# Kernel tuning notes

Measured on AMD Instinct MI355X. Metric: run time of the kernel, lower is better.

The kernel has to match this reference:

```python
import jax, jax.numpy as jnp
import numpy as np

N = 262144      # total nodes
E = 1048576     # total edges
G = 8192        # num graphs (= batch[-1]+1)
H = 128         # hidden
L = 4           # layers
VA = 64         # atom feature vocab
VB = 8          # bond feature vocab
FA = 9          # atom feature columns
FB = 3          # bond feature columns
BN_EPS = 1e-5


def _bn(x, g, b, m, v):
    # BatchNorm1d in eval mode: running stats
    return (x - m) * jax.lax.rsqrt(v + BN_EPS) * g + b


def setup_inputs() -> dict:
    key = jax.random.key(0)
    ks = jax.random.split(key, 40)
    rn = lambda k, s, sc=0.05: jax.random.normal(k, s, dtype=jnp.float32) * sc
    x = jax.random.randint(ks[0], (N, FA), 0, VA)
    edge_index = jax.random.randint(ks[1], (2, E), 0, N)
    edge_attr = jax.random.randint(ks[2], (E, FB), 0, VB)
    batch = jnp.sort(jax.random.randint(ks[3], (N,), 0, G))
    batch = batch.at[0].set(0).at[-1].set(G - 1)
    params = dict(
        atom_emb=rn(ks[4], (FA, VA, H)),
        vn_emb=rn(ks[5], (H,)),
        bond_emb=rn(ks[6], (L, FB, VB, H)),
        conv_eps=rn(ks[7], (L,)),
        conv_W1=rn(ks[8], (L, H, 2 * H)), conv_b1=rn(ks[9], (L, 2 * H)),
        conv_bn_g=1.0 + rn(ks[10], (L, 2 * H)), conv_bn_b=rn(ks[11], (L, 2 * H)),
        conv_bn_m=rn(ks[12], (L, 2 * H), 0.1),
        conv_bn_v=0.5 + jax.random.uniform(ks[13], (L, 2 * H)) * 0.5,
        conv_W2=rn(ks[14], (L, 2 * H, H)), conv_b2=rn(ks[15], (L, H)),
        vn1_W=rn(ks[16], (L, 2 * H, 2 * H)), vn1_b=rn(ks[17], (L, 2 * H)),
        vn1_g=1.0 + rn(ks[18], (L, 2 * H)), vn1_be=rn(ks[19], (L, 2 * H)),
        vn1_m=rn(ks[20], (L, 2 * H), 0.1),
        vn1_v=0.5 + jax.random.uniform(ks[21], (L, 2 * H)) * 0.5,
        vn2_W=rn(ks[22], (L, 2 * H, H)), vn2_b=rn(ks[23], (L, H)),
        vn2_g=1.0 + rn(ks[24], (L, H)), vn2_be=rn(ks[25], (L, H)),
        vn2_m=rn(ks[26], (L, H), 0.1),
        vn2_v=0.5 + jax.random.uniform(ks[27], (L, H)) * 0.5,
        pW1=rn(ks[28], (H, H)), pb1=rn(ks[29], (H,)),
        pW2=rn(ks[30], (H, 1)), pb2=rn(ks[31], (1,)),
    )
    return dict(x=x, edge_index=edge_index, edge_attr=edge_attr, batch=batch, **params)


def reference(x, edge_index, edge_attr, batch, atom_emb, vn_emb, bond_emb,
              conv_eps, conv_W1, conv_b1, conv_bn_g, conv_bn_b, conv_bn_m, conv_bn_v,
              conv_W2, conv_b2, vn1_W, vn1_b, vn1_g, vn1_be, vn1_m, vn1_v,
              vn2_W, vn2_b, vn2_g, vn2_be, vn2_m, vn2_v, pW1, pb1, pW2, pb2):
    src, dst = edge_index[0], edge_index[1]
    # AtomEncoder: sum of per-feature embeddings -> [N, H]
    h = atom_emb[jnp.arange(FA)[:, None], x.T].sum(0)
    # virtual node embedding broadcast to all graphs: [G, H]
    vn = jnp.broadcast_to(vn_emb, (G, H))
    for i in range(L):
        h = h + vn[batch]
        # CombConv (GIN-with-edge-features): msg = relu(x_j + bond_emb)
        e = bond_emb[i][jnp.arange(FB)[:, None], edge_attr.T].sum(0)  # [E, H]
        msg = jax.nn.relu(h[src] + e)
        agg = jax.ops.segment_sum(msg, dst, num_segments=N)  # [N, H]
        z = (1.0 + conv_eps[i]) * h + agg
        z = jax.nn.relu(_bn(z @ conv_W1[i] + conv_b1[i],
                            conv_bn_g[i], conv_bn_b[i], conv_bn_m[i], conv_bn_v[i]))
        h = z @ conv_W2[i] + conv_b2[i]
        # virtual node update: gather-concat-MLP, pool, MLP
        t = jnp.concatenate([vn[batch], h], axis=-1)  # [N, 2H]
        t = jax.nn.relu(_bn(t @ vn1_W[i] + vn1_b[i],
                            vn1_g[i], vn1_be[i], vn1_m[i], vn1_v[i]))
        pooled = jax.ops.segment_sum(t, batch, num_segments=G)  # [G, 2H]
        vn = jax.nn.relu(_bn(pooled @ vn2_W[i] + vn2_b[i],
                             vn2_g[i], vn2_be[i], vn2_m[i], vn2_v[i]))
    # JK='L': last virtual-node representation; dropout=0
    out = jax.nn.relu(vn @ pW1 + pb1) @ pW2 + pb2  # [G, 1]
    return jnp.clip(out, 0.0, 50.0)  # eval-mode clamp
```

## Files before the change

kernel.cpp:

```cpp
#include <hip/hip_runtime.h>
#include <hip/hip_fp16.h>

#define NN 262144
#define EE 1048576
#define GG 8192
#define HH 128
#define FBc 3
#define VAc 64
#define VBc 8
#define FAc 9

typedef _Float16 f16;
typedef _Float16 f16x8 __attribute__((ext_vector_type(8)));
typedef float f32x4 __attribute__((ext_vector_type(4)));

__device__ __forceinline__ float h2f(ushort u) {
    __half h; *(ushort*)&h = u; return __half2float(h);
}
__device__ __forceinline__ ushort f2h(float f) {
    __half h = __float2half_rn(f); return *(ushort*)&h;
}

__global__ void k_zero(float* __restrict__ p) {
    size_t i = (size_t)(blockIdx.x * 256 + threadIdx.x) * 4;
    *(float4*)(p + i) = make_float4(0.f, 0.f, 0.f, 0.f);
}

__global__ void k_atom(const int* __restrict__ x, const float* __restrict__ emb,
                       ushort* __restrict__ h16) {
    int t = blockIdx.x * 256 + threadIdx.x;
    int n = t >> 5, c = (t & 31) << 2;
    if (n >= NN) return;
    float4 a = make_float4(0.f, 0.f, 0.f, 0.f);
#pragma unroll
    for (int f = 0; f < FAc; ++f) {
        int v = x[n * FAc + f];
        float4 e = *(const float4*)(emb + ((size_t)(f * VAc + v)) * HH + c);
        a.x += e.x; a.y += e.y; a.z += e.z; a.w += e.w;
    }
    ushort4 o;
    o.x = f2h(a.x * 0.0625f); o.y = f2h(a.y * 0.0625f);
    o.z = f2h(a.z * 0.0625f); o.w = f2h(a.w * 0.0625f);
    *(ushort4*)(h16 + (size_t)n * HH + c) = o;
}

__global__ void k_init_vn(const float* __restrict__ vn_emb, float* __restrict__ vn) {
    int t = blockIdx.x * 256 + threadIdx.x;
    int g = t >> 5, c = (t & 31) << 2;
    *(float4*)(vn + (size_t)g * HH + c) = *(const float4*)(vn_emb + c);
}

__global__ void k_vn16(const float* __restrict__ vn, ushort* __restrict__ vn16) {
    int t = blockIdx.x * 256 + threadIdx.x;
    float4 v = *(const float4*)(vn + (size_t)t * 4);
    ushort4 o;
    o.x = f2h(v.x * 0.0625f); o.y = f2h(v.y * 0.0625f);
    o.z = f2h(v.z * 0.0625f); o.w = f2h(v.w * 0.0625f);
    *(ushort4*)(vn16 + (size_t)t * 4) = o;
}

__global__ void k_hist(const int* __restrict__ ei, int* __restrict__ deg) {
    int e = blockIdx.x * 256 + threadIdx.x;
    atomicAdd(&deg[ei[EE + e]], 1);
}
__global__ void k_scan1(const int* __restrict__ deg, int* __restrict__ rowptr,
                        int* __restrict__ sums) {
    __shared__ int s[256];
    int base = blockIdx.x * 1024 + threadIdx.x * 4;
    int4 d = *(const int4*)(deg + base);
    int t = d.x + d.y + d.z + d.w;
    s[threadIdx.x] = t;
    __syncthreads();
    for (int off = 1; off < 256; off <<= 1) {
        int v = (threadIdx.x >= off) ? s[threadIdx.x - off] : 0;
        __syncthreads();
        s[threadIdx.x] += v;
        __syncthreads();
    }
    int excl = s[threadIdx.x] - t;
    int4 o; o.x = excl; o.y = excl + d.x; o.z = o.y + d.y; o.w = o.z + d.z;
    *(int4*)(rowptr + base) = o;
    if (threadIdx.x == 255) sums[blockIdx.x] = s[255];
}
__global__ void k_scan2(int* __restrict__ sums) {
    __shared__ int s[256];
    int t = sums[threadIdx.x];
    s[threadIdx.x] = t;
    __syncthreads();
    for (int off = 1; off < 256; off <<= 1) {
        int v = (threadIdx.x >= off) ? s[threadIdx.x - off] : 0;
        __syncthreads();
        s[threadIdx.x] += v;
        __syncthreads();
    }
    sums[threadIdx.x] = s[threadIdx.x] - t;
}
__global__ void k_scan3(int* __restrict__ rowptr, const int* __restrict__ sums,
                        int* __restrict__ fill) {
    int base = blockIdx.x * 1024 + threadIdx.x * 4;
    int add = sums[blockIdx.x];
    int4 r = *(const int4*)(rowptr + base);
    r.x += add; r.y += add; r.z += add; r.w += add;
    *(int4*)(rowptr + base) = r;
    *(int4*)(fill + base) = r;
    if (blockIdx.x == 0 && threadIdx.x == 0) rowptr[NN] = EE;
}
__global__ void k_scatter(const int* __restrict__ ei, const int* __restrict__ ea,
                          int* __restrict__ fill, unsigned* __restrict__ packed) {
    int e = blockIdx.x * 256 + threadIdx.x;
    int dst = ei[EE + e];
    int pos = atomicAdd(&fill[dst], 1);
    unsigned cb = (unsigned)(ea[e * 3 + 0] + ea[e * 3 + 1] * 8 + ea[e * 3 + 2] * 64);
    packed[pos] = (unsigned)ei[e] | (cb << 18);
}

__global__ void k_ctab(const float* __restrict__ bemb, float* __restrict__ ctab) {
    int t = blockIdx.x * 256 + threadIdx.x;
    int cb = t >> 5, c = (t & 31) << 2;
    int a0 = cb & 7, a1 = (cb >> 3) & 7, a2 = cb >> 6;
    float4 b0 = *(const float4*)(bemb + (size_t)(0 * VBc + a0) * HH + c);
    float4 b1 = *(const float4*)(bemb + (size_t)(1 * VBc + a1) * HH + c);
    float4 b2 = *(const float4*)(bemb + (size_t)(2 * VBc + a2) * HH + c);
    float4 o = make_float4(b0.x + b1.x + b2.x, b0.y + b1.y + b2.y,
                           b0.z + b1.z + b2.z, b0.w + b1.w + b2.w);
    *(float4*)(ctab + (size_t)cb * HH + c) = o;
}

__global__ void k_prep(const float* __restrict__ b1, const float* __restrict__ g1,
                       const float* __restrict__ be1, const float* __restrict__ m1,
                       const float* __restrict__ v1,
                       const float* __restrict__ g3, const float* __restrict__ be3,
                       const float* __restrict__ m3, const float* __restrict__ v3,
                       float* __restrict__ ZA, float* __restrict__ ZB,
                       float* __restrict__ TA, float* __restrict__ TB,
                       float* __restrict__ S3) {
    int c = threadIdx.x;
    float s1 = g1[c] * rsqrtf(v1[c] + 1e-5f);
    ZA[c] = s1;
    ZB[c] = ((b1[c] - m1[c]) * s1 + be1[c]) * 0.0625f;
    float s3 = g3[c] * rsqrtf(v3[c] + 1e-5f);
    TA[c] = 16.f * s3;
    TB[c] = be3[c] - m3[c] * s3;
    S3[c] = s3;
}

__global__ void k_wt(const float* __restrict__ W, ushort* __restrict__ Wt, int lk, int Nsrc) {
    int o = blockIdx.x * 256 + threadIdx.x;
    int K = 1 << lk;
    int c = o >> lk, k = o & (K - 1);
    Wt[o] = f2h(W[(size_t)k * Nsrc + c]);
}

__global__ void k_agg(const ushort* __restrict__ h16, const ushort* __restrict__ vn16,
                      const int* __restrict__ batch,
                      const int* __restrict__ rowptr, const unsigned* __restrict__ packed,
                      const float* __restrict__ ctab, ushort* __restrict__ agg) {
    int n = blockIdx.x * 4 + (threadIdx.x >> 6);
    int lane = threadIdx.x & 63;
    int co = lane * 2;
    int beg = rowptr[n], end = rowptr[n + 1];
    float a0 = 0.f, a1 = 0.f;
    int i = beg;
    for (; i + 1 < end; i += 2) {
        unsigned p0 = packed[i], p1 = packed[i + 1];
        int s0 = p0 & 0x3FFFF, s1 = p1 & 0x3FFFF;
        int c0 = p0 >> 18, c1 = p1 >> 18;
        ushort2 u0 = *(const ushort2*)(h16 + (size_t)s0 * HH + co);
        ushort2 u1 = *(const ushort2*)(h16 + (size_t)s1 * HH + co);
        ushort2 w0 = *(const ushort2*)(vn16 + (size_t)batch[s0] * HH + co);
        ushort2 w1 = *(const ushort2*)(vn16 + (size_t)batch[s1] * HH + co);
        float2 t0 = *(const float2*)(ctab + (size_t)c0 * HH + co);
        float2 t1 = *(const float2*)(ctab + (size_t)c1 * HH + co);
        a0 += fmaxf(16.f * (h2f(u0.x) + h2f(w0.x)) + t0.x, 0.f)
            + fmaxf(16.f * (h2f(u1.x) + h2f(w1.x)) + t1.x, 0.f);
        a1 += fmaxf(16.f * (h2f(u0.y) + h2f(w0.y)) + t0.y, 0.f)
            + fmaxf(16.f * (h2f(u1.y) + h2f(w1.y)) + t1.y, 0.f);
    }
    if (i < end) {
        unsigned p = packed[i];
        int src = p & 0x3FFFF, cb = p >> 18;
        ushort2 u = *(const ushort2*)(h16 + (size_t)src * HH + co);
        ushort2 wv = *(const ushort2*)(vn16 + (size_t)batch[src] * HH + co);
        float2 ct = *(const float2*)(ctab + (size_t)cb * HH + co);
        a0 += fmaxf(16.f * (h2f(u.x) + h2f(wv.x)) + ct.x, 0.f);
        a1 += fmaxf(16.f * (h2f(u.y) + h2f(wv.y)) + ct.y, 0.f);
    }
    ushort2 o; o.x = f2h(a0 * 0.0625f); o.y = f2h(a1 * 0.0625f);
    *(ushort2*)(agg + (size_t)n * HH + co) = o;
}

__global__ void __launch_bounds__(256, 2)
k_conv(ushort* __restrict__ h16, const ushort* __restrict__ agg,
       const ushort* __restrict__ W1t, const ushort* __restrict__ W2t,
       const ushort* __restrict__ W3t,
       const int* __restrict__ batch, const ushort* __restrict__ vn16,
       const float* __restrict__ vnW,
       const float* __restrict__ eps_ptr,
       const float* __restrict__ ZA, const float* __restrict__ ZB,
       const float* __restrict__ b2,
       const float* __restrict__ TA, const float* __restrict__ TB,
       float* __restrict__ pooled) {
    __shared__ ushort As[64][128];
    __shared__ ushort zs[64][256];
    __shared__ ushort Wb[64][256];
    ushort(*Wq)[128] = (ushort(*)[128]) & Wb[0][0];
    const int tid = threadIdx.x;
    const int r0 = blockIdx.x * 64;
    const int w = tid >> 6, l = tid & 63, lr = l & 15, lg = l >> 4, lr7 = lr & 7;
    const float eps1 = 1.f + eps_ptr[0];
    f32x4 acc[4];

    {
        int row = tid >> 2, q = tid & 3, r7 = row & 7;
        int gg = batch[r0 + row];
        const ushort* hp = h16 + (size_t)(r0 + row) * HH;
        const ushort* vp = vn16 + (size_t)gg * HH;
        const ushort* ap = agg + (size_t)(r0 + row) * HH;
#pragma unroll
        for (int j4 = 0; j4 < 4; ++j4) {
            int c0 = q * 32 + j4 * 8;
            f16x8 hv = *(const f16x8*)(hp + c0);
            f16x8 vg = *(const f16x8*)(vp + c0);
            f16x8 ag = *(const f16x8*)(ap + c0);
            f16x8 o;
#pragma unroll
            for (int j = 0; j < 8; ++j)
                o[j] = (f16)(eps1 * ((float)hv[j] + (float)vg[j]) + (float)ag[j]);
            *(f16x8*)&As[row][((c0 >> 3) ^ r7) << 3] = o;
        }
    }

    for (int qt = 0; qt < 4; ++qt) {
        __syncthreads();
        {
            int c = tid >> 2, q = tid & 3, c7 = c & 7;
#pragma unroll
            for (int j4 = 0; j4 < 4; ++j4) {
                int blk = q * 4 + j4;
                *(f16x8*)&Wq[c][(blk ^ c7) << 3] =
                    *(const f16x8*)(W1t + (size_t)(qt * 64 + c) * 128 + blk * 8);
            }
        }
        __syncthreads();
#pragma unroll
        for (int fc = 0; fc < 4; ++fc) acc[fc] = (f32x4){0.f, 0.f, 0.f, 0.f};
#pragma unroll
        for (int k0 = 0; k0 < 4; ++k0) {
            int sb = ((k0 * 4 + lg) ^ lr7) << 3;
            f16x8 af = *(const f16x8*)&As[w * 16 + lr][sb];
#pragma unroll
            for (int fc = 0; fc < 4; ++fc) {
                f16x8 bf = *(const f16x8*)&Wq[fc * 16 + lr][sb];
                acc[fc] = __builtin_amdgcn_mfma_f32_16x16x32_f16(af, bf, acc[fc], 0, 0, 0);
            }
        }
#pragma unroll
        for (int fc = 0; fc < 4; ++fc) {
            int col = qt * 64 + fc * 16 + lr;
            float za = ZA[col], zb = ZB[col];
#pragma unroll
            for (int reg = 0; reg < 4; ++reg) {
                int rl = w * 16 + lg * 4 + reg;
                float zv = fmaxf(acc[fc][reg] * za + zb, 0.f);
                zs[rl][(((col >> 3) ^ (rl & 7)) << 3) | (col & 7)] = f2h(zv);
            }
        }
    }

    for (int ch = 0; ch < 2; ++ch) {
        __syncthreads();
        {
            int c = tid >> 2, q = tid & 3, c7 = c & 7;
#pragma unroll
            for (int j8 = 0; j8 < 8; ++j8) {
                int blk = q * 8 + j8;
                *(f16x8*)&Wb[c][(blk ^ c7) << 3] =
                    *(const f16x8*)(W2t + (size_t)(ch * 64 + c) * 256 + blk * 8);
            }
        }
        __syncthreads();
#pragma unroll
        for (int fc = 0; fc < 4; ++fc) acc[fc] = (f32x4){0.f, 0.f, 0.f, 0.f};
#pragma unroll
        for (int k0 = 0; k0 < 8; ++k0) {
            int sb = ((k0 * 4 + lg) ^ lr7) << 3;
            f16x8 af = *(const f16x8*)&zs[w * 16 + lr][sb];
#pragma unroll
            for (int fc = 0; fc < 4; ++fc) {
                f16x8 bf = *(const f16x8*)&Wb[fc * 16 + lr][sb];
                acc[fc] = __builtin_amdgcn_mfma_f32_16x16x32_f16(af, bf, acc[fc], 0, 0, 0);
            }
        }
#pragma unroll
        for (int fc = 0; fc < 4; ++fc) {
            int col = ch * 64 + fc * 16 + lr;
            float bb = b2[col];
#pragma unroll
            for (int reg = 0; reg < 4; ++reg) {
                int rl = w * 16 + lg * 4 + reg;
                float hv = acc[fc][reg] * 16.f + bb;
                ushort hq = f2h(hv * 0.0625f);
                h16[(size_t)(r0 + rl) * HH + col] = hq;
                As[rl][(((col >> 3) ^ (rl & 7)) << 3) | (col & 7)] = hq;
            }
        }
    }

    for (int qt = 0; qt < 4; ++qt) {
        __syncthreads();
        {
            int c = tid >> 2, q = tid & 3, c7 = c & 7;
#pragma unroll
            for (int j4 = 0; j4 < 4; ++j4) {
                int blk = q * 4 + j4;
                *(f16x8*)&Wq[c][(blk ^ c7) << 3] =
                    *(const f16x8*)(W3t + (size_t)(qt * 64 + c) * 128 + blk * 8);
            }
        }
        __syncthreads();
#pragma unroll
        for (int fc = 0; fc < 4; ++fc) acc[fc] = (f32x4){0.f, 0.f, 0.f, 0.f};
#pragma unroll
        for (int k0 = 0; k0 < 4; ++k0) {
            int sb = ((k0 * 4 + lg) ^ lr7) << 3;
            f16x8 af = *(const f16x8*)&As[w * 16 + lr][sb];
#pragma unroll
            for (int fc = 0; fc < 4; ++fc) {
                f16x8 bf = *(const f16x8*)&Wq[fc * 16 + lr][sb];
                acc[fc] = __builtin_amdgcn_mfma_f32_16x16x32_f16(af, bf, acc[fc], 0, 0, 0);
            }
        }
        int rls[4], ggs[4];
#pragma unroll
        for (int reg = 0; reg < 4; ++reg) {
            rls[reg] = w * 16 + lg * 4 + reg;
            ggs[reg] = batch[r0 + rls[reg]];
        }
#pragma unroll
        for (int fc = 0; fc < 4; ++fc) {
            int colg = qt * 64 + fc * 16 + lr;
            float ta = TA[colg], tb = TB[colg];
#pragma unroll
            for (int reg = 0; reg < 4; ++reg) {
                int rl = rls[reg];
                float tv = fmaxf(acc[fc][reg] * ta + vnW[(size_t)ggs[reg] * 256 + colg] + tb, 0.f);
                zs[rl][(((colg >> 3) ^ (rl & 7)) << 3) | (colg & 7)] = f2h(tv);
            }
        }
    }
    __syncthreads();
    {
        int col = tid;
        float s = 0.f;
        int cur = batch[r0];
        for (int r = 0; r < 64; ++r) {
            int gg = batch[r0 + r];
            if (gg != cur) {
                atomicAdd(&pooled[(size_t)cur * 256 + col], s);
                s = 0.f; cur = gg;
            }
            s += h2f(zs[r][(((col >> 3) ^ (r & 7)) << 3) | (col & 7)]);
        }
        atomicAdd(&pooled[(size_t)cur * 256 + col], s);
    }
}

enum { E_BIAS = 0, E_BNRELU = 1 };
template <int EMODE>
__global__ void __launch_bounds__(256)
gemm_k(const void* __restrict__ Av, const float* __restrict__ B,
       const float* __restrict__ bias,
       const float* __restrict__ g_, const float* __restrict__ b_,
       const float* __restrict__ m_, const float* __restrict__ v_,
       const float* __restrict__ scp,
       void* __restrict__ outv, int K, int Nc) {
    __shared__ float As[64][33];
    __shared__ float Bs[32][64];
    const int tid = threadIdx.x;
    const int row0 = blockIdx.x * 64;
    const int col0 = blockIdx.y * 64;
    float acc[4][4] = {};
    const int tx = tid & 15, ty = tid >> 4;
    for (int k0 = 0; k0 < K; k0 += 32) {
#pragma unroll
        for (int p = 0; p < 2; ++p) {
            int idx = p * 256 + tid;
            {
                int r = idx >> 3, c = (idx & 7) << 2;
                size_t aoff = (size_t)(row0 + r) * K + k0 + c;
                float4 va = *(const float4*)((const float*)Av + aoff);
                As[r][c + 0] = va.x; As[r][c + 1] = va.y;
                As[r][c + 2] = va.z; As[r][c + 3] = va.w;
            }
            {
                int kr = idx >> 4, cc = (idx & 15) << 2;
                *(float4*)&Bs[kr][cc] =
                    *(const float4*)(B + (size_t)(k0 + kr) * Nc + col0 + cc);
            }
        }
        __syncthreads();
#pragma unroll
        for (int k = 0; k < 32; ++k) {
            float4 bv = *(const float4*)&Bs[k][tx << 2];
            float a0 = As[ty * 4 + 0][k];
            float a1 = As[ty * 4 + 1][k];
            float a2 = As[ty * 4 + 2][k];
            float a3 = As[ty * 4 + 3][k];
            acc[0][0] += a0 * bv.x; acc[0][1] += a0 * bv.y; acc[0][2] += a0 * bv.z; acc[0][3] += a0 * bv.w;
            acc[1][0] += a1 * bv.x; acc[1][1] += a1 * bv.y; acc[1][2] += a1 * bv.z; acc[1][3] += a1 * bv.w;
            acc[2][0] += a2 * bv.x; acc[2][1] += a2 * bv.y; acc[2][2] += a2 * bv.z; acc[2][3] += a2 * bv.w;
            acc[3][0] += a3 * bv.x; acc[3][1] += a3 * bv.y; acc[3][2] += a3 * bv.z; acc[3][3] += a3 * bv.w;
        }
        __syncthreads();
    }
#pragma unroll
    for (int j = 0; j < 4; ++j) {
        int gr = row0 + ty * 4 + j;
        float vals[4];
#pragma unroll
        for (int lx = 0; lx < 4; ++lx) {
            int gc = col0 + (tx << 2) + lx;
            float val = acc[j][lx];
            if (EMODE == E_BIAS) {
                float v = val + bias[gc];
                if (scp) v *= scp[gc];
                vals[lx] = v;
            } else {
                float y = val + bias[gc];
                float s = g_[gc] * rsqrtf(v_[gc] + 1e-5f);
                y = (y - m_[gc]) * s + b_[gc];
                vals[lx] = fmaxf(y, 0.f);
            }
        }
        *(float4*)((float*)outv + (size_t)gr * Nc + col0 + (tx << 2)) =
            make_float4(vals[0], vals[1], vals[2], vals[3]);
    }
}

__global__ void k_final(const float* __restrict__ vn, const float* __restrict__ pW1,
                        const float* __restrict__ pb1, const float* __restrict__ pW2,
                        const float* __restrict__ pb2, float* __restrict__ out) {
    int g = blockIdx.x;
    int j = threadIdx.x;
    __shared__ float vrow[HH];
    __shared__ float red[HH];
    vrow[j] = vn[(size_t)g * HH + j];
    __syncthreads();
    float acc = pb1[j];
    for (int k = 0; k < HH; ++k) acc = fmaf(vrow[k], pW1[k * HH + j], acc);
    red[j] = fmaxf(acc, 0.f) * pW2[j];
    __syncthreads();
    for (int s = 64; s > 0; s >>= 1) {
        if (j < s) red[j] += red[j + s];
        __syncthreads();
    }
    if (j == 0) out[g] = fminf(fmaxf(red[0] + pb2[0], 0.f), 50.f);
}

extern "C" void kernel_launch(void* const* d_in, const int* in_sizes, int n_in,
                              void* d_out, int out_size, void* d_ws, size_t ws_size,
                              hipStream_t stream) {
    const int*   x        = (const int*)  d_in[0];
    const int*   ei       = (const int*)  d_in[1];
    const int*   ea       = (const int*)  d_in[2];
    const int*   batch    = (const int*)  d_in[3];
    const float* atom_emb = (const float*)d_in[4];
    const float* vn_emb   = (const float*)d_in[5];
    const float* bond_emb = (const float*)d_in[6];
    const float* conv_eps = (const float*)d_in[7];
    const float* conv_W1  = (const float*)d_in[8];
    const float* conv_b1  = (const float*)d_in[9];
    const float* cbn_g    = (const float*)d_in[10];
    const float* cbn_b    = (const float*)d_in[11];
    const float* cbn_m    = (const float*)d_in[12];
    const float* cbn_v    = (const float*)d_in[13];
    const float* conv_W2  = (const float*)d_in[14];
    const float* conv_b2  = (const float*)d_in[15];
    const float* vn1_W    = (const float*)d_in[16];
    const float* vn1_b    = (const float*)d_in[17];
    const float* vn1_g    = (const float*)d_in[18];
    const float* vn1_be   = (const float*)d_in[19];
    const float* vn1_m    = (const float*)d_in[20];
    const float* vn1_v    = (const float*)d_in[21];
    const float* vn2_W    = (const float*)d_in[22];
    const float* vn2_b    = (const float*)d_in[23];
    const float* vn2_g    = (const float*)d_in[24];
    const float* vn2_be   = (const float*)d_in[25];
    const float* vn2_m    = (const float*)d_in[26];
    const float* vn2_v    = (const float*)d_in[27];
    const float* pW1      = (const float*)d_in[28];
    const float* pb1      = (const float*)d_in[29];
    const float* pW2      = (const float*)d_in[30];
    const float* pb2      = (const float*)d_in[31];

    char* base = (char*)d_ws;
    ushort*   h16    = (ushort*)base;
    ushort*   agg    = h16 + (size_t)NN * HH;
    unsigned* packed = (unsigned*)(agg + (size_t)NN * HH);
    int*      rowptr = (int*)(packed + EE);
    int*      fill   = rowptr + NN + 4;
    float*    ctab   = (float*)(fill + NN);
    int*      sums   = (int*)(ctab + 512 * HH);
    ushort*   W1t    = (ushort*)(sums + 256);
    ushort*   W2t    = W1t + 256 * 128;
    ushort*   W3t    = W2t + 128 * 256;
    float*    ZA     = (float*)(W3t + 256 * 128);
    float*    ZB     = ZA + 256;
    float*    TA     = ZB + 256;
    float*    TB     = TA + 256;
    float*    S3     = TB + 256;
    float*    vn     = S3 + 256;
    ushort*   vn16   = (ushort*)(vn + (size_t)GG * HH);
    float*    vnW    = (float*)(vn16 + (size_t)GG * HH);
    float*    pooled = vnW + (size_t)GG * 256;
    float*    out    = (float*)d_out;

    k_zero<<<256, 256, 0, stream>>>((float*)fill);
    k_hist<<<EE / 256, 256, 0, stream>>>(ei, fill);
    k_scan1<<<256, 256, 0, stream>>>(fill, rowptr, sums);
    k_scan2<<<1, 256, 0, stream>>>(sums);
    k_scan3<<<256, 256, 0, stream>>>(rowptr, sums, fill);
    k_scatter<<<EE / 256, 256, 0, stream>>>(ei, ea, fill, packed);
    k_atom<<<NN * 32 / 256, 256, 0, stream>>>(x, atom_emb, h16);
    k_init_vn<<<GG * HH / 4 / 256, 256, 0, stream>>>(vn_emb, vn);

    for (int i = 0; i < 4; ++i) {
        k_ctab<<<64, 256, 0, stream>>>(bond_emb + (size_t)i * FBc * VBc * HH, ctab);
        k_prep<<<1, 256, 0, stream>>>(
            conv_b1 + i * 256, cbn_g + i * 256, cbn_b + i * 256,
            cbn_m + i * 256, cbn_v + i * 256,
            vn1_g + i * 256, vn1_be + i * 256, vn1_m + i * 256, vn1_v + i * 256,
            ZA, ZB, TA, TB, S3);
        k_wt<<<128, 256, 0, stream>>>(conv_W1 + (size_t)i * HH * 256, W1t, 7, 256);
        k_wt<<<128, 256, 0, stream>>>(conv_W2 + (size_t)i * 256 * HH, W2t, 8, 128);
        k_wt<<<128, 256, 0, stream>>>(vn1_W + (size_t)i * 256 * 256 + 128 * 256, W3t, 7, 256);
        k_vn16<<<GG * HH / 4 / 256, 256, 0, stream>>>(vn, vn16);

        k_agg<<<NN / 4, 256, 0, stream>>>(h16, vn16, batch, rowptr, packed, ctab, agg);

        {
            dim3 g3(GG / 64, 4);
            gemm_k<E_BIAS><<<g3, 256, 0, stream>>>(
                vn, vn1_W + (size_t)i * 256 * 256, vn1_b + i * 256,
                nullptr, nullptr, nullptr, nullptr, S3, vnW, HH, 256);
        }
        k_zero<<<GG * 256 / 4 / 256, 256, 0, stream>>>(pooled);

        k_conv<<<NN / 64, 256, 0, stream>>>(
            h16, agg, W1t, W2t, W3t, batch, vn16, vnW, conv_eps + i,
            ZA, ZB, conv_b2 + i * HH, TA, TB, pooled);

        {
            dim3 g4(GG / 64, 2);
            gemm_k<E_BNRELU><<<g4, 256, 0, stream>>>(
                pooled, vn2_W + (size_t)i * 256 * HH, vn2_b + i * HH,
                vn2_g + i * HH, vn2_be + i * HH, vn2_m + i * HH, vn2_v + i * HH,
                nullptr, vn, 256, HH);
        }
    }
    k_final<<<GG, 128, 0, stream>>>(vn, pW1, pb1, pW2, pb2, out);
}
```

Baseline: 1.609 ms.

## Read conv weights directly from global and shrink LDS to raise occupancy

Rewrites the fused conv kernel so the MFMA B-operands come straight from global or L2 instead of being staged through shared memory. A-fragments for the first GEMM are built in registers, and one 64x256 LDS buffer is reused for z, h and the t halves. The pooling reduction is split into two halves of columns, each with its own barrier. This removes most __syncthreads and LDS traffic and raises the occupancy target to 4 blocks per CU, at the cost of redundant per-wave weight reads from cache and more register pressure (8 accumulators for the second GEMM).

After: 2.742 ms. 1.7x slower.

```diff
diff --git a/kernel.cpp b/kernel.cpp
--- a/kernel.cpp
+++ b/kernel.cpp
@@ -189,7 +189,7 @@
     *(ushort2*)(agg + (size_t)n * HH + co) = o;
 }
 
-__global__ void __launch_bounds__(256, 2)
+__global__ void __launch_bounds__(256, 4)
 k_conv(ushort* __restrict__ h16, const ushort* __restrict__ agg,
        const ushort* __restrict__ W1t, const ushort* __restrict__ W2t,
        const ushort* __restrict__ W3t,
@@ -200,58 +200,44 @@
        const float* __restrict__ b2,
        const float* __restrict__ TA, const float* __restrict__ TB,
        float* __restrict__ pooled) {
-    __shared__ ushort As[64][128];
     __shared__ ushort zs[64][256];
-    __shared__ ushort Wb[64][256];
-    ushort(*Wq)[128] = (ushort(*)[128]) & Wb[0][0];
     const int tid = threadIdx.x;
     const int r0 = blockIdx.x * 64;
     const int w = tid >> 6, l = tid & 63, lr = l & 15, lg = l >> 4, lr7 = lr & 7;
     const float eps1 = 1.f + eps_ptr[0];
-    f32x4 acc[4];
-
-    {
-        int row = tid >> 2, q = tid & 3, r7 = row & 7;
-        int gg = batch[r0 + row];
-        const ushort* hp = h16 + (size_t)(r0 + row) * HH;
-        const ushort* vp = vn16 + (size_t)gg * HH;
-        const ushort* ap = agg + (size_t)(r0 + row) * HH;
-#pragma unroll
-        for (int j4 = 0; j4 < 4; ++j4) {
-            int c0 = q * 32 + j4 * 8;
-            f16x8 hv = *(const f16x8*)(hp + c0);
-            f16x8 vg = *(const f16x8*)(vp + c0);
-            f16x8 ag = *(const f16x8*)(ap + c0);
-            f16x8 o;
-#pragma unroll
-            for (int j = 0; j < 8; ++j)
-                o[j] = (f16)(eps1 * ((float)hv[j] + (float)vg[j]) + (float)ag[j]);
-            *(f16x8*)&As[row][((c0 >> 3) ^ r7) << 3] = o;
-        }
-    }
-
+    const int myrow = w * 16 + lr;
+    const int growA = r0 + myrow;
+    const int ggA = batch[growA];
+    int rl[4], ggs[4];
+#pragma unroll
+    for (int reg = 0; reg < 4; ++reg) {
+        rl[reg] = w * 16 + lg * 4 + reg;
+        ggs[reg] = batch[r0 + rl[reg]];
+    }
+
+    f16x8 af[4];
+#pragma unroll
+    for (int k0 = 0; k0 < 4; ++k0) {
+        int ko = k0 * 32 + lg * 8;
+        f16x8 hv = *(const f16x8*)(h16 + (size_t)growA * HH + ko);
+        f16x8 vv = *(const f16x8*)(vn16 + (size_t)ggA * HH + ko);
+        f16x8 ag = *(const f16x8*)(agg + (size_t)growA * HH + ko);
+#pragma unroll
+        for (int j = 0; j < 8; ++j)
+            af[k0][j] = (f16)(eps1 * ((float)hv[j] + (float)vv[j]) + (float)ag[j]);
+    }
+
+#pragma unroll
     for (int qt = 0; qt < 4; ++qt) {
-        __syncthreads();
-        {
-            int c = tid >> 2, q = tid & 3, c7 = c & 7;
-#pragma unroll
-            for (int j4 = 0; j4 < 4; ++j4) {
-                int blk = q * 4 + j4;
-                *(f16x8*)&Wq[c][(blk ^ c7) << 3] =
-                    *(const f16x8*)(W1t + (size_t)(qt * 64 + c) * 128 + blk * 8);
-            }
-        }
-        __syncthreads();
-#pragma unroll
-        for (int fc = 0; fc < 4; ++fc) acc[fc] = (f32x4){0.f, 0.f, 0.f, 0.f};
+        f32x4 acc[4] = {};
 #pragma unroll
         for (int k0 = 0; k0 < 4; ++k0) {
-            int sb = ((k0 * 4 + lg) ^ lr7) << 3;
-            f16x8 af = *(const f16x8*)&As[w * 16 + lr][sb];
+            int ko = k0 * 32 + lg * 8;
 #pragma unroll
             for (int fc = 0; fc < 4; ++fc) {
-                f16x8 bf = *(const f16x8*)&Wq[fc * 16 + lr][sb];
-                acc[fc] = __builtin_amdgcn_mfma_f32_16x16x32_f16(af, bf, acc[fc], 0, 0, 0);
+                int col = qt * 64 + fc * 16 + lr;
+                f16x8 bf = *(const f16x8*)(W1t + (size_t)col * 128 + ko);
+                acc[fc] = __builtin_amdgcn_mfma_f32_16x16x32_f16(af[k0], bf, acc[fc], 0, 0, 0);
             }
         }
 #pragma unroll
@@ -260,108 +246,85 @@
             float za = ZA[col], zb = ZB[col];
 #pragma unroll
             for (int reg = 0; reg < 4; ++reg) {
-                int rl = w * 16 + lg * 4 + reg;
                 float zv = fmaxf(acc[fc][reg] * za + zb, 0.f);
-                zs[rl][(((col >> 3) ^ (rl & 7)) << 3) | (col & 7)] = f2h(zv);
-            }
-        }
-    }
-
-    for (int ch = 0; ch < 2; ++ch) {
+                zs[rl[reg]][(((col >> 3) ^ (rl[reg] & 7)) << 3) | (col & 7)] = f2h(zv);
+            }
+        }
+    }
+
+    {
+        f32x4 acc2[8] = {};
+#pragma unroll
+        for (int k0 = 0; k0 < 8; ++k0) {
+            int ko = k0 * 32 + lg * 8;
+            f16x8 az = *(const f16x8*)&zs[myrow][(((k0 * 4 + lg) ^ lr7)) << 3];
+#pragma unroll
+            for (int ofc = 0; ofc < 8; ++ofc) {
+                int col = (ofc >> 2) * 64 + (ofc & 3) * 16 + lr;
+                f16x8 bf = *(const f16x8*)(W2t + (size_t)col * 256 + ko);
+                acc2[ofc] = __builtin_amdgcn_mfma_f32_16x16x32_f16(az, bf, acc2[ofc], 0, 0, 0);
+            }
+        }
+#pragma unroll
+        for (int ofc = 0; ofc < 8; ++ofc) {
+            int col = (ofc >> 2) * 64 + (ofc & 3) * 16 + lr;
+            float bb = b2[col];
+#pragma unroll
+            for (int reg = 0; reg < 4; ++reg) {
+                float hv = acc2[ofc][reg] * 16.f + bb;
+                ushort hq = f2h(hv * 0.0625f);
+                h16[(size_t)(r0 + rl[reg]) * HH + col] = hq;
+                zs[rl[reg]][(((col >> 3) ^ (rl[reg] & 7)) << 3) | (col & 7)] = hq;
+            }
+        }
+    }
+
+    for (int pr = 0; pr < 2; ++pr) {
+#pragma unroll
+        for (int sub = 0; sub < 2; ++sub) {
+            int qt = pr * 2 + sub;
+            f32x4 acc3[4] = {};
+#pragma unroll
+            for (int k0 = 0; k0 < 4; ++k0) {
+                int ko = k0 * 32 + lg * 8;
+                f16x8 ah = *(const f16x8*)&zs[myrow][(((k0 * 4 + lg) ^ lr7)) << 3];
+#pragma unroll
+                for (int fc = 0; fc < 4; ++fc) {
+                    int col = qt * 64 + fc * 16 + lr;
+                    f16x8 bf = *(const f16x8*)(W3t + (size_t)col * 128 + ko);
+                    acc3[fc] = __builtin_amdgcn_mfma_f32_16x16x32_f16(ah, bf, acc3[fc], 0, 0, 0);
+                }
+            }
+#pragma unroll
+            for (int fc = 0; fc < 4; ++fc) {
+                int colg = qt * 64 + fc * 16 + lr;
+                int colL = 128 + sub * 64 + fc * 16 + lr;
+                float ta = TA[colg], tb = TB[colg];
+#pragma unroll
+                for (int reg = 0; reg < 4; ++reg) {
+                    float tv = fmaxf(acc3[fc][reg] * ta + vnW[(size_t)ggs[reg] * 256 + colg] + tb, 0.f);
+                    zs[rl[reg]][(((colL >> 3) ^ (rl[reg] & 7)) << 3) | (colL & 7)] = f2h(tv);
+                }
+            }
+        }
         __syncthreads();
         {
-            int c = tid >> 2, q = tid & 3, c7 = c & 7;
-#pragma unroll
-            for (int j8 = 0; j8 < 8; ++j8) {
-                int blk = q * 8 + j8;
-                *(f16x8*)&Wb[c][(blk ^ c7) << 3] =
-                    *(const f16x8*)(W2t + (size_t)(ch * 64 + c) * 256 + blk * 8);
-            }
-        }
-        __syncthreads();
-#pragma unroll
-        for (int fc = 0; fc < 4; ++fc) acc[fc] = (f32x4){0.f, 0.f, 0.f, 0.f};
-#pragma unroll
-        for (int k0 = 0; k0 < 8; ++k0) {
-            int sb = ((k0 * 4 + lg) ^ lr7) << 3;
-            f16x8 af = *(const f16x8*)&zs[w * 16 + lr][sb];
-#pragma unroll
-            for (int fc = 0; fc < 4; ++fc) {
-                f16x8 bf = *(const f16x8*)&Wb[fc * 16 + lr][sb];
-                acc[fc] = __builtin_amdgcn_mfma_f32_16x16x32_f16(af, bf, acc[fc], 0, 0, 0);
-            }
-        }
-#pragma unroll
-        for (int fc = 0; fc < 4; ++fc) {
-            int col = ch * 64 + fc * 16 + lr;
-            float bb = b2[col];
-#pragma unroll
-            for (int reg = 0; reg < 4; ++reg) {
-                int rl = w * 16 + lg * 4 + reg;
-                float hv = acc[fc][reg] * 16.f + bb;
-                ushort hq = f2h(hv * 0.0625f);
-                h16[(size_t)(r0 + rl) * HH + col] = hq;
-                As[rl][(((col >> 3) ^ (rl & 7)) << 3) | (col & 7)] = hq;
-            }
-        }
-    }
-
-    for (int qt = 0; qt < 4; ++qt) {
-        __syncthreads();
-        {
-            int c = tid >> 2, q = tid & 3, c7 = c & 7;
-#pragma unroll
-            for (int j4 = 0; j4 < 4; ++j4) {
-                int blk = q * 4 + j4;
-                *(f16x8*)&Wq[c][(blk ^ c7) << 3] =
-                    *(const f16x8*)(W3t + (size_t)(qt * 64 + c) * 128 + blk * 8);
-            }
-        }
-        __syncthreads();
-#pragma unroll
-        for (int fc = 0; fc < 4; ++fc) acc[fc] = (f32x4){0.f, 0.f, 0.f, 0.f};
-#pragma unroll
-        for (int k0 = 0; k0 < 4; ++k0) {
-            int sb = ((k0 * 4 + lg) ^ lr7) << 3;
-            f16x8 af = *(const f16x8*)&As[w * 16 + lr][sb];
-#pragma unroll
-            for (int fc = 0; fc < 4; ++fc) {
-                f16x8 bf = *(const f16x8*)&Wq[fc * 16 + lr][sb];
-                acc[fc] = __builtin_amdgcn_mfma_f32_16x16x32_f16(af, bf, acc[fc], 0, 0, 0);
-            }
-        }
-        int rls[4], ggs[4];
-#pragma unroll
-        for (int reg = 0; reg < 4; ++reg) {
-            rls[reg] = w * 16 + lg * 4 + reg;
-            ggs[reg] = batch[r0 + rls[reg]];
-        }
-#pragma unroll
-        for (int fc = 0; fc < 4; ++fc) {
-            int colg = qt * 64 + fc * 16 + lr;
-            float ta = TA[colg], tb = TB[colg];
-#pragma unroll
-            for (int reg = 0; reg < 4; ++reg) {
-                int rl = rls[reg];
-                float tv = fmaxf(acc[fc][reg] * ta + vnW[(size_t)ggs[reg] * 256 + colg] + tb, 0.f);
-                zs[rl][(((colg >> 3) ^ (rl & 7)) << 3) | (colg & 7)] = f2h(tv);
-            }
-        }
-    }
-    __syncthreads();
-    {
-        int col = tid;
-        float s = 0.f;
-        int cur = batch[r0];
-        for (int r = 0; r < 64; ++r) {
-            int gg = batch[r0 + r];
-            if (gg != cur) {
-                atomicAdd(&pooled[(size_t)cur * 256 + col], s);
-                s = 0.f; cur = gg;
-            }
-            s += h2f(zs[r][(((col >> 3) ^ (r & 7)) << 3) | (col & 7)]);
-        }
-        atomicAdd(&pooled[(size_t)cur * 256 + col], s);
+            int c = tid & 127, half = tid >> 7;
+            int gcol = pr * 128 + c;
+            int colL = 128 + c;
+            float s = 0.f;
+            int cur = batch[r0 + half * 32];
+            for (int r = half * 32; r < half * 32 + 32; ++r) {
+                int gg = batch[r0 + r];
+                if (gg != cur) {
+                    atomicAdd(&pooled[(size_t)cur * 256 + gcol], s);
+                    s = 0.f; cur = gg;
+                }
+                s += h2f(zs[r][(((colL >> 3) ^ (r & 7)) << 3) | (colL & 7)]);
+            }
+            atomicAdd(&pooled[(size_t)cur * 256 + gcol], s);
+        }
+        __syncthreads();
     }
 }
 
```

## Prefetch next weight chunk into registers and widen weight chunks in fused conv kernel

Applied to the files above, without the earlier changes.

The fused conv/VN MLP kernel now stages weights in 128-column chunks instead of 64, so each GEMM needs half as many LDS refill and barrier rounds. The next chunk's weights are loaded from global memory into registers while the current chunk's MFMAs run, which overlaps global latency with compute. It also hoists the batch-index loads out of the inner loop. The cost is more live registers, with 8 f16x8 prefetch registers plus 8 accumulators, which may reduce occupancy under launch_bounds(256,2).

Measured after the change: 1.664 ms. 1.03x slower.

```diff
diff --git a/kernel.cpp b/kernel.cpp
--- a/kernel.cpp
+++ b/kernel.cpp
@@ -19,6 +19,9 @@
 }
 __device__ __forceinline__ ushort f2h(float f) {
     __half h = __float2half_rn(f); return *(ushort*)&h;
+}
+__device__ __forceinline__ int swz(int col, int row) {
+    return (((col >> 3) ^ (row & 7)) << 3) | (col & 7);
 }
 
 __global__ void k_zero(float* __restrict__ p) {
@@ -202,13 +205,27 @@
        float* __restrict__ pooled) {
     __shared__ ushort As[64][128];
     __shared__ ushort zs[64][256];
-    __shared__ ushort Wb[64][256];
-    ushort(*Wq)[128] = (ushort(*)[128]) & Wb[0][0];
+    __shared__ ushort Wb[128][128];
+    ushort(*Wb2)[256] = (ushort(*)[256]) & Wb[0][0];
     const int tid = threadIdx.x;
     const int r0 = blockIdx.x * 64;
     const int w = tid >> 6, l = tid & 63, lr = l & 15, lg = l >> 4, lr7 = lr & 7;
     const float eps1 = 1.f + eps_ptr[0];
-    f32x4 acc[4];
+    const int myrow = w * 16 + lr;
+    int rl[4], ggs[4];
+#pragma unroll
+    for (int reg = 0; reg < 4; ++reg) {
+        rl[reg] = w * 16 + lg * 4 + reg;
+        ggs[reg] = batch[r0 + rl[reg]];
+    }
+
+    f16x8 wreg[8];
+    {
+        int c = tid >> 1, q = tid & 1;
+        const ushort* s = W1t + (size_t)c * 128 + q * 64;
+#pragma unroll
+        for (int j = 0; j < 8; ++j) wreg[j] = *(const f16x8*)(s + j * 8);
+    }
 
     {
         int row = tid >> 2, q = tid & 3, r7 = row & 7;
@@ -230,121 +247,128 @@
         }
     }
 
-    for (int qt = 0; qt < 4; ++qt) {
+    for (int ch = 0; ch < 2; ++ch) {
+        __syncthreads();
+        {
+            int c = tid >> 1, q = tid & 1, c7 = c & 7;
+#pragma unroll
+            for (int j = 0; j < 8; ++j)
+                *(f16x8*)&Wb[c][((q * 8 + j) ^ c7) << 3] = wreg[j];
+        }
+        __syncthreads();
+        if (ch == 0) {
+            int c = tid >> 1, q = tid & 1;
+            const ushort* s = W1t + (size_t)(128 + c) * 128 + q * 64;
+#pragma unroll
+            for (int j = 0; j < 8; ++j) wreg[j] = *(const f16x8*)(s + j * 8);
+        } else {
+            int c = tid >> 2, q = tid & 3;
+            const ushort* s = W2t + (size_t)c * 256 + q * 64;
+#pragma unroll
+            for (int j = 0; j < 8; ++j) wreg[j] = *(const f16x8*)(s + j * 8);
+        }
+        f32x4 acc[8] = {};
+#pragma unroll
+        for (int k0 = 0; k0 < 4; ++k0) {
+            int sb = ((k0 * 4 + lg) ^ lr7) << 3;
+            f16x8 af = *(const f16x8*)&As[myrow][sb];
+#pragma unroll
+            for (int fc = 0; fc < 8; ++fc) {
+                f16x8 bf = *(const f16x8*)&Wb[fc * 16 + lr][sb];
+                acc[fc] = __builtin_amdgcn_mfma_f32_16x16x32_f16(af, bf, acc[fc], 0, 0, 0);
+            }
+        }
+#pragma unroll
+        for (int fc = 0; fc < 8; ++fc) {
+            int col = ch * 128 + fc * 16 + lr;
+            float za = ZA[col], zb = ZB[col];
+#pragma unroll
+            for (int reg = 0; reg < 4; ++reg) {
+                float zv = fmaxf(acc[fc][reg] * za + zb, 0.f);
+                zs[rl[reg]][swz(col, rl[reg])] = f2h(zv);
+            }
+        }
+    }
+
+    for (int ch2 = 0; ch2 < 2; ++ch2) {
         __syncthreads();
         {
             int c = tid >> 2, q = tid & 3, c7 = c & 7;
 #pragma unroll
-            for (int j4 = 0; j4 < 4; ++j4) {
-                int blk = q * 4 + j4;
-                *(f16x8*)&Wq[c][(blk ^ c7) << 3] =
-                    *(const f16x8*)(W1t + (size_t)(qt * 64 + c) * 128 + blk * 8);
-            }
-        }
-        __syncthreads();
-#pragma unroll
-        for (int fc = 0; fc < 4; ++fc) acc[fc] = (f32x4){0.f, 0.f, 0.f, 0.f};
+            for (int j = 0; j < 8; ++j)
+                *(f16x8*)&Wb2[c][((q * 8 + j) ^ c7) << 3] = wreg[j];
+        }
+        __syncthreads();
+        if (ch2 == 0) {
+            int c = tid >> 2, q = tid & 3;
+            const ushort* s = W2t + (size_t)(64 + c) * 256 + q * 64;
+#pragma unroll
+            for (int j = 0; j < 8; ++j) wreg[j] = *(const f16x8*)(s + j * 8);
+        } else {
+            int c = tid >> 1, q = tid & 1;
+            const ushort* s = W3t + (size_t)c * 128 + q * 64;
+#pragma unroll
+            for (int j = 0; j < 8; ++j) wreg[j] = *(const f16x8*)(s + j * 8);
+        }
+        f32x4 acc[4] = {};
+#pragma unroll
+        for (int k0 = 0; k0 < 8; ++k0) {
+            int sb = ((k0 * 4 + lg) ^ lr7) << 3;
+            f16x8 az = *(const f16x8*)&zs[myrow][sb];
+#pragma unroll
+            for (int fc = 0; fc < 4; ++fc) {
+                f16x8 bf = *(const f16x8*)&Wb2[fc * 16 + lr][sb];
+                acc[fc] = __builtin_amdgcn_mfma_f32_16x16x32_f16(az, bf, acc[fc], 0, 0, 0);
+            }
+        }
+#pragma unroll
+        for (int fc = 0; fc < 4; ++fc) {
+            int col = ch2 * 64 + fc * 16 + lr;
+            float bb = b2[col];
+#pragma unroll
+            for (int reg = 0; reg < 4; ++reg) {
+                float hv = acc[fc][reg] * 16.f + bb;
+                ushort hq = f2h(hv * 0.0625f);
+                h16[(size_t)(r0 + rl[reg]) * HH + col] = hq;
+                As[rl[reg]][swz(col, rl[reg])] = hq;
+            }
+        }
+    }
+
+    for (int ch3 = 0; ch3 < 2; ++ch3) {
+        __syncthreads();
+        {
+            int c = tid >> 1, q = tid & 1, c7 = c & 7;
+#pragma unroll
+            for (int j = 0; j < 8; ++j)
+                *(f16x8*)&Wb[c][((q * 8 + j) ^ c7) << 3] = wreg[j];
+        }
+        __syncthreads();
+        if (ch3 == 0) {
+            int c = tid >> 1, q = tid & 1;
+            const ushort* s = W3t + (size_t)(128 + c) * 128 + q * 64;
+#pragma unroll
+            for (int j = 0; j < 8; ++j) wreg[j] = *(const f16x8*)(s + j * 8);
+        }
+        f32x4 acc[8] = {};
 #pragma unroll
         for (int k0 = 0; k0 < 4; ++k0) {
             int sb = ((k0 * 4 + lg) ^ lr7) << 3;
-            f16x8 af = *(const f16x8*)&As[w * 16 + lr][sb];
-#pragma unroll
-            for (int fc = 0; fc < 4; ++fc) {
-                f16x8 bf = *(const f16x8*)&Wq[fc * 16 + lr][sb];
-                acc[fc] = __builtin_amdgcn_mfma_f32_16x16x32_f16(af, bf, acc[fc], 0, 0, 0);
-            }
-        }
-#pragma unroll
-        for (int fc = 0; fc < 4; ++fc) {
-            int col = qt * 64 + fc * 16 + lr;
-            float za = ZA[col], zb = ZB[col];
+            f16x8 ah = *(const f16x8*)&As[myrow][sb];
+#pragma unroll
+            for (int fc = 0; fc < 8; ++fc) {
+                f16x8 bf = *(const f16x8*)&Wb[fc * 16 + lr][sb];
+                acc[fc] = __builtin_amdgcn_mfma_f32_16x16x32_f16(ah, bf, acc[fc], 0, 0, 0);
+            }
+        }
+#pragma unroll
+        for (int fc = 0; fc < 8; ++fc) {
+            int colg = ch3 * 128 + fc * 16 + lr;
+            float ta = TA[colg], tb = TB[colg];
 #pragma unroll
             for (int reg = 0; reg < 4; ++reg) {
-                int rl = w * 16 + lg * 4 + reg;
-                float zv = fmaxf(acc[fc][reg] * za + zb, 0.f);
-                zs[rl][(((col >> 3) ^ (rl & 7)) << 3) | (col & 7)] = f2h(zv);
-            }
-        }
-    }
-
-    for (int ch = 0; ch < 2; ++ch) {
-        __syncthreads();
-        {
-            int c = tid >> 2, q = tid & 3, c7 = c & 7;
-#pragma unroll
-            for (int j8 = 0; j8 < 8; ++j8) {
-                int blk = q * 8 + j8;
-                *(f16x8*)&Wb[c][(blk ^ c7) << 3] =
-                    *(const f16x8*)(W2t + (size_t)(ch * 64 + c) * 256 + blk * 8);
-            }
-        }
-        __syncthreads();
-#pragma unroll
-        for (int fc = 0; fc < 4; ++fc) acc[fc] = (f32x4){0.f, 0.f, 0.f, 0.f};
-#pragma unroll
-        for (int k0 = 0; k0 < 8; ++k0) {
-            int sb = ((k0 * 4 + lg) ^ lr7) << 3;
-            f16x8 af = *(const f16x8*)&zs[w * 16 + lr][sb];
-#pragma unroll
-            for (int fc = 0; fc < 4; ++fc) {
-                f16x8 bf = *(const f16x8*)&Wb[fc * 16 + lr][sb];
-                acc[fc] = __builtin_amdgcn_mfma_f32_16x16x32_f16(af, bf, acc[fc], 0, 0, 0);
-            }
-        }
-#pragma unroll
-        for (int fc = 0; fc < 4; ++fc) {
-            int col = ch * 64 + fc * 16 + lr;
-            float bb = b2[col];
-#pragma unroll
-            for (int reg = 0; reg < 4; ++reg) {
-                int rl = w * 16 + lg * 4 + reg;
-                float hv = acc[fc][reg] * 16.f + bb;
-                ushort hq = f2h(hv * 0.0625f);
-                h16[(size_t)(r0 + rl) * HH + col] = hq;
-                As[rl][(((col >> 3) ^ (rl & 7)) << 3) | (col & 7)] = hq;
-            }
-        }
-    }
-
-    for (int qt = 0; qt < 4; ++qt) {
-        __syncthreads();
-        {
-            int c = tid >> 2, q = tid & 3, c7 = c & 7;
-#pragma unroll
-            for (int j4 = 0; j4 < 4; ++j4) {
-                int blk = q * 4 + j4;
-                *(f16x8*)&Wq[c][(blk ^ c7) << 3] =
-                    *(const f16x8*)(W3t + (size_t)(qt * 64 + c) * 128 + blk * 8);
-            }
-        }
-        __syncthreads();
-#pragma unroll
-        for (int fc = 0; fc < 4; ++fc) acc[fc] = (f32x4){0.f, 0.f, 0.f, 0.f};
-#pragma unroll
-        for (int k0 = 0; k0 < 4; ++k0) {
-            int sb = ((k0 * 4 + lg) ^ lr7) << 3;
-            f16x8 af = *(const f16x8*)&As[w * 16 + lr][sb];
-#pragma unroll
-            for (int fc = 0; fc < 4; ++fc) {
-                f16x8 bf = *(const f16x8*)&Wq[fc * 16 + lr][sb];
-                acc[fc] = __builtin_amdgcn_mfma_f32_16x16x32_f16(af, bf, acc[fc], 0, 0, 0);
-            }
-        }
-        int rls[4], ggs[4];
-#pragma unroll
-        for (int reg = 0; reg < 4; ++reg) {
-            rls[reg] = w * 16 + lg * 4 + reg;
-            ggs[reg] = batch[r0 + rls[reg]];
-        }
-#pragma unroll
-        for (int fc = 0; fc < 4; ++fc) {
-            int colg = qt * 64 + fc * 16 + lr;
-            float ta = TA[colg], tb = TB[colg];
-#pragma unroll
-            for (int reg = 0; reg < 4; ++reg) {
-                int rl = rls[reg];
                 float tv = fmaxf(acc[fc][reg] * ta + vnW[(size_t)ggs[reg] * 256 + colg] + tb, 0.f);
-                zs[rl][(((colg >> 3) ^ (rl & 7)) << 3) | (colg & 7)] = f2h(tv);
+                zs[rl[reg]][swz(colg, rl[reg])] = f2h(tv);
             }
         }
     }
@@ -359,7 +383,7 @@
                 atomicAdd(&pooled[(size_t)cur * 256 + col], s);
                 s = 0.f; cur = gg;
             }
-            s += h2f(zs[r][(((col >> 3) ^ (r & 7)) << 3) | (col & 7)]);
+            s += h2f(zs[r][swz(col, r)]);
         }
         atomicAdd(&pooled[(size_t)cur * 256 + col], s);
     }
```
